# Kernel optimization log

Hardware: AMD Instinct MI355X
Metric: run time of the kernel (lower is better)

The kernel has to match this reference:

```python
import jax, jax.numpy as jnp
import numpy as np

LOG_CLAMP = -100.0  # torch BCE clamps log terms at -100


def _weights_from_target(target):
    # target: [B, 1, W, W]; weight[b,i,j] = W / (sqrt((i-x)^2 + (j-y)^2) + 1)
    # where (x, y) is the mean location of the per-sample max of target.
    B = target.shape[0]
    W = target.shape[-1]
    t = target.reshape(B, W, W)
    m = jnp.max(t, axis=(1, 2), keepdims=True)
    mask = (t == m).astype(t.dtype)                      # all argmax locations
    cnt = jnp.sum(mask, axis=(1, 2))                     # [B]
    idx = jnp.arange(W, dtype=t.dtype)
    x = jnp.sum(mask * idx[None, :, None], axis=(1, 2)) / cnt  # mean row index
    y = jnp.sum(mask * idx[None, None, :], axis=(1, 2)) / cnt  # mean col index
    a = idx[None, :, None] - x[:, None, None]            # [B, W, 1]
    b = idx[None, None, :] - y[:, None, None]            # [B, 1, W]
    dist = (jnp.sqrt(a * a + b * b) + 1.0) / W           # [B, W, W]
    return (1.0 / dist).reshape(target.shape)


def reference(input, target):
    weights = _weights_from_target(target)
    log_p = jnp.maximum(jnp.log(input), LOG_CLAMP)
    log_1mp = jnp.maximum(jnp.log1p(-input), LOG_CLAMP)
    bce = -(target * log_p + (1.0 - target) * log_1mp)
    return jnp.mean(weights * bce)


def setup_inputs() -> dict:
    key = jax.random.key(0)
    k1, k2 = jax.random.split(key)
    shape = (256, 1, 224, 224)
    # BCE requires probabilities in (0,1); keep strictly inside via small margin.
    input = jax.random.uniform(k1, shape, dtype=jnp.float32, minval=1e-4, maxval=1.0 - 1e-4)
    target = jax.random.uniform(k2, shape, dtype=jnp.float32)
    return {"input": input, "target": target}
```

## Files before the change

### kernel.cpp

```cpp
#include <hip/hip_runtime.h>
#include <math.h>


#define WIMG 224
#define WW (WIMG * WIMG)
#define NQ (WW / 4)
#define NB 256
#define K1_THREADS 1024
#define NPARTB 4
#define QPB (NQ / NPARTB)
#define K2_THREADS 512
#define NPART (NB * NPARTB)
#define LN2 0.69314718055994530942f
#define CLAMP2 (-144.269504088896340736f)

__global__ __launch_bounds__(K1_THREADS) void centroid_kernel(
    const float* __restrict__ target, float* __restrict__ xy)
{
    const int b   = blockIdx.x;
    const int tid = threadIdx.x;
    const float4* __restrict__ t4 = (const float4*)(target + (size_t)b * WW);

    float m = -1.0f, cnt = 0.0f, si = 0.0f, sj = 0.0f;
    for (int q = tid; q < NQ; q += K1_THREADS) {
        float4 v = t4[q];
        int i  = q / 56;
        int j0 = (q - i * 56) * 4;
        float fi = (float)i;
        float vv[4] = {v.x, v.y, v.z, v.w};
        #pragma unroll
        for (int k = 0; k < 4; ++k) {
            float val = vv[k];
            float fj  = (float)(j0 + k);
            bool gt = val > m;
            bool eq = val == m;
            cnt = gt ? 1.0f : (cnt + (eq ? 1.0f : 0.0f));
            si  = gt ? fi   : (si  + (eq ? fi   : 0.0f));
            sj  = gt ? fj   : (sj  + (eq ? fj   : 0.0f));
            m   = fmaxf(m, val);
        }
    }
    #pragma unroll
    for (int off = 32; off > 0; off >>= 1) {
        float m2  = __shfl_down(m,   off);
        float c2  = __shfl_down(cnt, off);
        float si2 = __shfl_down(si,  off);
        float sj2 = __shfl_down(sj,  off);
        bool gt = m2 > m, eq = m2 == m;
        cnt = gt ? c2  : (cnt + (eq ? c2  : 0.0f));
        si  = gt ? si2 : (si  + (eq ? si2 : 0.0f));
        sj  = gt ? sj2 : (sj  + (eq ? sj2 : 0.0f));
        m   = fmaxf(m, m2);
    }
    __shared__ float sm[16], sc[16], ssi[16], ssj[16];
    const int lane = tid & 63, wid = tid >> 6;
    if (lane == 0) { sm[wid] = m; sc[wid] = cnt; ssi[wid] = si; ssj[wid] = sj; }
    __syncthreads();
    if (tid == 0) {
        float M = sm[0], C = sc[0], SI = ssi[0], SJ = ssj[0];
        #pragma unroll
        for (int w = 1; w < 16; ++w) {
            float mw = sm[w];
            bool gt = mw > M, eq = mw == M;
            C  = gt ? sc[w]  : (C  + (eq ? sc[w]  : 0.0f));
            SI = gt ? ssi[w] : (SI + (eq ? ssi[w] : 0.0f));
            SJ = gt ? ssj[w] : (SJ + (eq ? ssj[w] : 0.0f));
            M  = fmaxf(M, mw);
        }
        xy[2 * b]     = SI / C;
        xy[2 * b + 1] = SJ / C;
    }
}

__global__ __launch_bounds__(K2_THREADS) void bce_kernel(
    const float* __restrict__ input,
    const float* __restrict__ target,
    const float* __restrict__ xy,
    float* __restrict__ partial)
{
    const int blk  = blockIdx.x;
    const int b    = blk >> 2;
    const int part = blk & 3;
    const int tid  = threadIdx.x;
    const float x = xy[2 * b];
    const float y = xy[2 * b + 1];
    const float4* __restrict__ t4 = (const float4*)(target + (size_t)b * WW);
    const float4* __restrict__ p4 = (const float4*)(input  + (size_t)b * WW);
    const int qbase = part * QPB;
    const float Kc = -(float)WIMG * LN2;

    float acc = 0.0f;
    for (int ql = tid; ql < QPB; ql += K2_THREADS) {
        int q  = qbase + ql;
        float4 tv = t4[q];
        float4 pv = p4[q];
        int i  = q / 56;
        int j0 = (q - i * 56) * 4;
        float di  = (float)i - x;
        float di2 = di * di;
        float tt[4] = {tv.x, tv.y, tv.z, tv.w};
        float pp[4] = {pv.x, pv.y, pv.z, pv.w};
        #pragma unroll
        for (int k = 0; k < 4; ++k) {
            float dj = (float)(j0 + k) - y;
            float s  = __builtin_amdgcn_sqrtf(di2 + dj * dj);
            float wf = Kc * __builtin_amdgcn_rcpf(s + 1.0f);
            float p = pp[k], t = tt[k];
            float lp2  = fmaxf(__builtin_amdgcn_logf(p),        CLAMP2);
            float l1p2 = fmaxf(__builtin_amdgcn_logf(1.0f - p), CLAMP2);
            acc += wf * (l1p2 + t * (lp2 - l1p2));
        }
    }
    #pragma unroll
    for (int off = 32; off > 0; off >>= 1) acc += __shfl_down(acc, off);
    __shared__ float sred[8];
    const int lane = tid & 63, wid = tid >> 6;
    if (lane == 0) sred[wid] = acc;
    __syncthreads();
    if (tid == 0) {
        float ssum = 0.0f;
        #pragma unroll
        for (int w = 0; w < 8; ++w) ssum += sred[w];
        partial[blk] = ssum;
    }
}

__global__ __launch_bounds__(NPART) void final_reduce(
    const float* __restrict__ partial, float* __restrict__ out, float inv_total)
{
    const int tid = threadIdx.x;
    float v = partial[tid];
    #pragma unroll
    for (int off = 32; off > 0; off >>= 1) v += __shfl_down(v, off);
    __shared__ float sred[16];
    const int lane = tid & 63, wid = tid >> 6;
    if (lane == 0) sred[wid] = v;
    __syncthreads();
    if (tid == 0) {
        float s = 0.0f;
        #pragma unroll
        for (int w = 0; w < 16; ++w) s += sred[w];
        out[0] = s * inv_total;
    }
}

extern "C" void kernel_launch(void* const* d_in, const int* in_sizes, int n_in,
                              void* d_out, int out_size, void* d_ws, size_t ws_size,
                              hipStream_t stream) {
    const float* input  = (const float*)d_in[0];
    const float* target = (const float*)d_in[1];
    float* out = (float*)d_out;
    float* xy      = (float*)d_ws;
    float* partial = (float*)d_ws + 512;

    centroid_kernel<<<NB, K1_THREADS, 0, stream>>>(target, xy);
    bce_kernel<<<NPART, K2_THREADS, 0, stream>>>(input, target, xy, partial);
    const float inv_total = 1.0f / (256.0f * 224.0f * 224.0f);
    final_reduce<<<1, NPART, 0, stream>>>(partial, out, inv_total);
}
```

Before: 125.3 us.

## Split centroid pass across four blocks per sample and fold final reduce into atomics

The centroid pass now runs 1024 blocks (four per sample) instead of 256, each writing partial max/count/index sums that the BCE kernel merges at its start. Both kernels use 448 threads so the 3136 quads per part divide exactly and the loops fully unroll. The separate final-reduce kernel is replaced by per-block atomicAdd into the output, which needs a memset node first. This aims to raise occupancy in the first pass and cut a launch, at the cost of a memset and nondeterministic float summation order.

```diff
diff --git a/kernel.cpp b/kernel.cpp
--- a/kernel.cpp
+++ b/kernel.cpp
@@ -6,23 +6,27 @@
 #define WW (WIMG * WIMG)
 #define NQ (WW / 4)
 #define NB 256
-#define K1_THREADS 1024
 #define NPARTB 4
 #define QPB (NQ / NPARTB)
-#define K2_THREADS 512
-#define NPART (NB * NPARTB)
+#define NTHR 448
+#define NBLK (NB * NPARTB)
 #define LN2 0.69314718055994530942f
 #define CLAMP2 (-144.269504088896340736f)
 
-__global__ __launch_bounds__(K1_THREADS) void centroid_kernel(
-    const float* __restrict__ target, float* __restrict__ xy)
+__global__ __launch_bounds__(NTHR) void stats_kernel(
+    const float* __restrict__ target, float4* __restrict__ stats)
 {
-    const int b   = blockIdx.x;
-    const int tid = threadIdx.x;
+    const int blk  = blockIdx.x;
+    const int b    = blk >> 2;
+    const int part = blk & 3;
+    const int tid  = threadIdx.x;
     const float4* __restrict__ t4 = (const float4*)(target + (size_t)b * WW);
+    const int qbase = part * QPB;
 
     float m = -1.0f, cnt = 0.0f, si = 0.0f, sj = 0.0f;
-    for (int q = tid; q < NQ; q += K1_THREADS) {
+    #pragma unroll
+    for (int it = 0; it < QPB / NTHR; ++it) {
+        int q  = qbase + it * NTHR + tid;
         float4 v = t4[q];
         int i  = q / 56;
         int j0 = (q - i * 56) * 4;
@@ -52,14 +56,14 @@
         sj  = gt ? sj2 : (sj  + (eq ? sj2 : 0.0f));
         m   = fmaxf(m, m2);
     }
-    __shared__ float sm[16], sc[16], ssi[16], ssj[16];
+    __shared__ float sm[7], sc[7], ssi[7], ssj[7];
     const int lane = tid & 63, wid = tid >> 6;
     if (lane == 0) { sm[wid] = m; sc[wid] = cnt; ssi[wid] = si; ssj[wid] = sj; }
     __syncthreads();
     if (tid == 0) {
         float M = sm[0], C = sc[0], SI = ssi[0], SJ = ssj[0];
         #pragma unroll
-        for (int w = 1; w < 16; ++w) {
+        for (int w = 1; w < 7; ++w) {
             float mw = sm[w];
             bool gt = mw > M, eq = mw == M;
             C  = gt ? sc[w]  : (C  + (eq ? sc[w]  : 0.0f));
@@ -67,31 +71,50 @@
             SJ = gt ? ssj[w] : (SJ + (eq ? ssj[w] : 0.0f));
             M  = fmaxf(M, mw);
         }
-        xy[2 * b]     = SI / C;
-        xy[2 * b + 1] = SJ / C;
+        stats[blk] = make_float4(M, C, SI, SJ);
     }
 }
 
-__global__ __launch_bounds__(K2_THREADS) void bce_kernel(
+__global__ __launch_bounds__(NTHR) void bce_kernel(
     const float* __restrict__ input,
     const float* __restrict__ target,
-    const float* __restrict__ xy,
-    float* __restrict__ partial)
+    const float4* __restrict__ stats,
+    float* __restrict__ out,
+    float inv_total)
 {
     const int blk  = blockIdx.x;
     const int b    = blk >> 2;
     const int part = blk & 3;
     const int tid  = threadIdx.x;
-    const float x = xy[2 * b];
-    const float y = xy[2 * b + 1];
+
+    __shared__ float sxy[2];
+    if (tid == 0) {
+        float4 s0 = stats[b * 4];
+        float M = s0.x, C = s0.y, SI = s0.z, SJ = s0.w;
+        #pragma unroll
+        for (int t = 1; t < 4; ++t) {
+            float4 s = stats[b * 4 + t];
+            bool gt = s.x > M, eq = s.x == M;
+            C  = gt ? s.y : (C  + (eq ? s.y : 0.0f));
+            SI = gt ? s.z : (SI + (eq ? s.z : 0.0f));
+            SJ = gt ? s.w : (SJ + (eq ? s.w : 0.0f));
+            M  = fmaxf(M, s.x);
+        }
+        sxy[0] = SI / C;
+        sxy[1] = SJ / C;
+    }
+    __syncthreads();
+    const float x = sxy[0], y = sxy[1];
+
     const float4* __restrict__ t4 = (const float4*)(target + (size_t)b * WW);
     const float4* __restrict__ p4 = (const float4*)(input  + (size_t)b * WW);
     const int qbase = part * QPB;
     const float Kc = -(float)WIMG * LN2;
 
     float acc = 0.0f;
-    for (int ql = tid; ql < QPB; ql += K2_THREADS) {
-        int q  = qbase + ql;
+    #pragma unroll
+    for (int it = 0; it < QPB / NTHR; ++it) {
+        int q  = qbase + it * NTHR + tid;
         float4 tv = t4[q];
         float4 pv = p4[q];
         int i  = q / 56;
@@ -113,34 +136,15 @@
     }
     #pragma unroll
     for (int off = 32; off > 0; off >>= 1) acc += __shfl_down(acc, off);
-    __shared__ float sred[8];
+    __shared__ float sred[7];
     const int lane = tid & 63, wid = tid >> 6;
     if (lane == 0) sred[wid] = acc;
     __syncthreads();
     if (tid == 0) {
         float ssum = 0.0f;
         #pragma unroll
-        for (int w = 0; w < 8; ++w) ssum += sred[w];
-        partial[blk] = ssum;
-    }
-}
-
-__global__ __launch_bounds__(NPART) void final_reduce(
-    const float* __restrict__ partial, float* __restrict__ out, float inv_total)
-{
-    const int tid = threadIdx.x;
-    float v = partial[tid];
-    #pragma unroll
-    for (int off = 32; off > 0; off >>= 1) v += __shfl_down(v, off);
-    __shared__ float sred[16];
-    const int lane = tid & 63, wid = tid >> 6;
-    if (lane == 0) sred[wid] = v;
-    __syncthreads();
-    if (tid == 0) {
-        float s = 0.0f;
-        #pragma unroll
-        for (int w = 0; w < 16; ++w) s += sred[w];
-        out[0] = s * inv_total;
+        for (int w = 0; w < 7; ++w) ssum += sred[w];
+        atomicAdd(out, ssum * inv_total);
     }
 }
 
@@ -150,11 +154,10 @@
     const float* input  = (const float*)d_in[0];
     const float* target = (const float*)d_in[1];
     float* out = (float*)d_out;
-    float* xy      = (float*)d_ws;
-    float* partial = (float*)d_ws + 512;
+    float4* stats = (float4*)d_ws;
 
-    centroid_kernel<<<NB, K1_THREADS, 0, stream>>>(target, xy);
-    bce_kernel<<<NPART, K2_THREADS, 0, stream>>>(input, target, xy, partial);
+    hipMemsetAsync(out, 0, sizeof(float), stream);
+    stats_kernel<<<NBLK, NTHR, 0, stream>>>(target, stats);
     const float inv_total = 1.0f / (256.0f * 224.0f * 224.0f);
-    final_reduce<<<1, NPART, 0, stream>>>(partial, out, inv_total);
+    bce_kernel<<<NBLK, NTHR, 0, stream>>>(input, target, stats, out, inv_total);
 }
```

Result: slower. 129.7 us (+3.5%).
